# Optimization experiments

Hardware: AMD Instinct MI355X
Metric: run time of the kernel (lower is better)

## Reference

```python
import jax, jax.numpy as jnp
import numpy as np


def setup_inputs() -> dict:
    key = jax.random.key(0)
    ks = jax.random.split(key, 12)
    B, T, E, H, D, NB, BS = 64, 1, 1280, 20, 64, 7, 64
    w = lambda k: jax.random.normal(k, (E, E), jnp.float32) * 0.02
    return {
        "hidden_states": jax.random.normal(ks[0], (B, T, E), jnp.float32),
        "kcache": jax.random.normal(ks[1], (B, H, NB, BS, D), jnp.float32),
        "vcache": jax.random.normal(ks[2], (B, H, NB, BS, D), jnp.float32),
        "wq": w(ks[3]), "bq": jax.random.normal(ks[4], (E,), jnp.float32) * 0.02,
        "wk": w(ks[5]), "bk": jnp.zeros((E,), jnp.float32),
        "wv": w(ks[6]), "bv": jax.random.normal(ks[7], (E,), jnp.float32) * 0.02,
        "wo": w(ks[8]), "bo": jax.random.normal(ks[9], (E,), jnp.float32) * 0.02,
        "cache_position": jax.random.randint(ks[10], (B,), 0, 447, jnp.int32),
        "block_tables": jax.random.randint(ks[11], (B, NB), 0, NB, jnp.int32),
    }


def reference(hidden_states, kcache, vcache, wq, bq, wk, bk, wv, bv, wo, bo,
              cache_position, block_tables):
    B, T, E = hidden_states.shape          # T == 1 (decode)
    _, H, NB, BS, D = kcache.shape
    L = NB * BS                             # max logical cache length (448)
    scaling = D ** -0.5

    # projections -> (B, H, T, D)
    q = (hidden_states @ wq.T + bq).reshape(B, T, H, D).transpose(0, 2, 1, 3) * scaling
    kn = (hidden_states @ wk.T + bk).reshape(B, T, H, D).transpose(0, 2, 1, 3)
    vn = (hidden_states @ wv.T + bv).reshape(B, T, H, D).transpose(0, 2, 1, 3)

    # paged block-table gather: logical cache (B, H, L, D)
    bt = block_tables[:, None, :, None, None].astype(jnp.int32)
    kc = jnp.take_along_axis(kcache, bt, axis=2).reshape(B, H, L, D)
    vc = jnp.take_along_axis(vcache, bt, axis=2).reshape(B, H, L, D)

    # insert the new token's k/v at position cache_position[b]
    pos = jnp.arange(L, dtype=jnp.int32)
    seq = cache_position.reshape(B, 1, 1, 1)
    at_new = pos.reshape(1, 1, L, 1) == seq          # (B,1,L,1)
    k_full = jnp.where(at_new, kn, kc)               # kn (B,H,1,D) broadcasts
    v_full = jnp.where(at_new, vn, vc)

    # causal decode: attend to positions <= cache_position
    scores = jnp.einsum('bhtd,bhld->bhtl', q, k_full)
    valid = pos.reshape(1, 1, 1, L) <= cache_position.reshape(B, 1, 1, 1)
    scores = jnp.where(valid, scores, jnp.finfo(scores.dtype).min)
    probs = jax.nn.softmax(scores, axis=-1)
    out = jnp.einsum('bhtl,bhld->bhtd', probs, v_full)

    out = out.transpose(0, 2, 1, 3).reshape(B, T, E)
    return out @ wo.T + bo
```

## Files before the change

kernel.cpp:

```cpp
#include <hip/hip_runtime.h>
#include <math.h>

#define E 1280
#define NHEAD 20
#define HD 64
#define NBLK 7
#define NB 64

typedef __bf16 bf16x8 __attribute__((ext_vector_type(8)));
typedef __bf16 bf16x4 __attribute__((ext_vector_type(4)));
typedef float floatx4 __attribute__((ext_vector_type(4)));

__device__ __forceinline__ float wave_max64(float v) {
    #pragma unroll
    for (int o = 32; o > 0; o >>= 1) v = fmaxf(v, __shfl_xor(v, o, 64));
    return v;
}
__device__ __forceinline__ float wave_sum64(float v) {
    #pragma unroll
    for (int o = 32; o > 0; o >>= 1) v += __shfl_xor(v, o, 64);
    return v;
}

__device__ __forceinline__ bf16x4 cvt4(float4 v) {
    bf16x4 p;
    p[0] = (__bf16)v.x; p[1] = (__bf16)v.y; p[2] = (__bf16)v.z; p[3] = (__bf16)v.w;
    return p;
}

template<int NTOT, bool QKV>
__global__ __launch_bounds__(256) void mfma_gemm(
    const float* __restrict__ A,
    const float* __restrict__ W0, const float* __restrict__ W1,
    const float* __restrict__ W2,
    const float* __restrict__ b0, const float* __restrict__ b1,
    const float* __restrict__ b2,
    float* __restrict__ C)
{
    __shared__ __align__(16) __bf16 Asl[4][64][72];
    __shared__ __align__(16) __bf16 Wsl[4][16][72];

    const int t = threadIdx.x;
    const int lane = t & 63;
    const int wv = t >> 6;
    const int quad = lane >> 4;
    const int l16 = lane & 15;
    const int jg0 = blockIdx.x * 16;

    int j0; const float* Wp; const float* bp; float scl;
    if (QKV) {
        const int msel = jg0 / E;
        j0 = jg0 - msel * E;
        Wp = (msel == 0) ? W0 : ((msel == 1) ? W1 : W2);
        bp = (msel == 0) ? b0 : ((msel == 1) ? b1 : b2);
        scl = (msel == 0) ? 0.125f : 1.0f;
    } else { j0 = jg0; Wp = W0; bp = b0; scl = 1.0f; }

    const int sr = lane >> 2;
    const int sc = lane & 3;

    floatx4 acc[4] = {};

    const int kbeg = wv * (E / 4);
    for (int c = 0; c < 5; ++c) {
        const int k0 = kbeg + c * 64;
        #pragma unroll
        for (int rg = 0; rg < 4; ++rg) {
            #pragma unroll
            for (int cg = 0; cg < 4; ++cg) {
                float4 v = *(const float4*)&A[(size_t)(rg * 16 + sr) * E + k0 + cg * 16 + sc * 4];
                *(bf16x4*)&Asl[wv][rg * 16 + sr][cg * 16 + sc * 4] = cvt4(v);
            }
        }
        #pragma unroll
        for (int cg = 0; cg < 4; ++cg) {
            float4 v = *(const float4*)&Wp[(size_t)(j0 + sr) * E + k0 + cg * 16 + sc * 4];
            *(bf16x4*)&Wsl[wv][sr][cg * 16 + sc * 4] = cvt4(v);
        }
        bf16x8 bfr0 = *(const bf16x8*)&Wsl[wv][l16][quad * 8];
        bf16x8 bfr1 = *(const bf16x8*)&Wsl[wv][l16][32 + quad * 8];
        #pragma unroll
        for (int rg = 0; rg < 4; ++rg) {
            bf16x8 af0 = *(const bf16x8*)&Asl[wv][rg * 16 + l16][quad * 8];
            acc[rg] = __builtin_amdgcn_mfma_f32_16x16x32_bf16(af0, bfr0, acc[rg], 0, 0, 0);
            bf16x8 af1 = *(const bf16x8*)&Asl[wv][rg * 16 + l16][32 + quad * 8];
            acc[rg] = __builtin_amdgcn_mfma_f32_16x16x32_bf16(af1, bfr1, acc[rg], 0, 0, 0);
        }
    }

    __syncthreads();
    float (*Cred)[64][16] = (float (*)[64][16])&Asl[0][0][0];
    #pragma unroll
    for (int r = 0; r < 4; ++r) {
        #pragma unroll
        for (int rg = 0; rg < 4; ++rg)
            ;
        ;
    }
    #pragma unroll
    for (int rg = 0; rg < 4; ++rg) {
        #pragma unroll
        for (int r = 0; r < 4; ++r)
            Cred[wv][rg * 16 + quad * 4 + r][l16] = acc[rg][r];
    }
    __syncthreads();

    #pragma unroll
    for (int i = 0; i < 4; ++i) {
        const int e = t + i * 256;
        const int row = e >> 4, col = e & 15;
        float s = Cred[0][row][col] + Cred[1][row][col]
                + Cred[2][row][col] + Cred[3][row][col];
        C[(size_t)row * NTOT + jg0 + col] = (s + bp[j0 + col]) * scl;
    }
}

__global__ __launch_bounds__(256) void attn_kernel(
    const float* __restrict__ qkv,
    const float* __restrict__ kcache, const float* __restrict__ vcache,
    const int* __restrict__ cache_position, const int* __restrict__ block_tables,
    float* __restrict__ obuf)
{
    const int bh = blockIdx.x;
    const int b = bh / NHEAD;
    const int h = bh % NHEAD;
    const int lane = threadIdx.x & 63;
    const int wv = threadIdx.x >> 6;
    const int d4 = lane & 15;
    const int sg = lane >> 4;

    __shared__ __align__(16) float q_lds[64];
    __shared__ __align__(16) float o_lds[4][64];
    __shared__ float ml_lds[4][2];

    const int pos = cache_position[b];
    const int last = pos - 1;
    const int col = h * HD + lane;

    const float qd  = qkv[(size_t)b * (3 * E) + col];
    const float knd = qkv[(size_t)b * (3 * E) + E + col];
    const float vnd = qkv[(size_t)b * (3 * E) + 2 * E + col];
    if (wv == 0) q_lds[lane] = qd;
    __syncthreads();

    float m = -INFINITY, lsum = 0.0f;
    float4 vacc = make_float4(0.f, 0.f, 0.f, 0.f);

    for (int nb = wv; nb * 64 <= last; nb += 4) {
        const int phys = block_tables[b * NBLK + nb];
        const size_t boff = ((size_t)((b * NHEAD + h) * NBLK + phys)) << 12;
        const float* __restrict__ Kb = kcache + boff;
        const float* __restrict__ Vb = vcache + boff;

        float sc = 0.0f;
        const float4* Krow = (const float4*)(Kb + lane * HD);
        #pragma unroll
        for (int dd = 0; dd < 16; ++dd) {
            float4 k4 = Krow[dd];
            float4 q4 = ((const float4*)q_lds)[dd];
            sc = fmaf(k4.x, q4.x, sc);
            sc = fmaf(k4.y, q4.y, sc);
            sc = fmaf(k4.z, q4.z, sc);
            sc = fmaf(k4.w, q4.w, sc);
        }
        const int l = nb * 64 + lane;
        if (l > last) sc = -INFINITY;

        const float bm = wave_max64(sc);
        const float mnew = fmaxf(m, bm);
        const float alpha = __expf(m - mnew);
        const float p = __expf(sc - mnew);
        lsum = lsum * alpha + wave_sum64(p);
        vacc.x *= alpha; vacc.y *= alpha; vacc.z *= alpha; vacc.w *= alpha;

        #pragma unroll
        for (int j = 0; j < 16; ++j) {
            const int s = sg + 4 * j;
            const float ps = __shfl(p, s, 64);
            float4 v4 = *(const float4*)&Vb[s * HD + d4 * 4];
            vacc.x = fmaf(ps, v4.x, vacc.x);
            vacc.y = fmaf(ps, v4.y, vacc.y);
            vacc.z = fmaf(ps, v4.z, vacc.z);
            vacc.w = fmaf(ps, v4.w, vacc.w);
        }
        m = mnew;
    }

    #pragma unroll
    for (int o = 16; o <= 32; o <<= 1) {
        vacc.x += __shfl_xor(vacc.x, o, 64);
        vacc.y += __shfl_xor(vacc.y, o, 64);
        vacc.z += __shfl_xor(vacc.z, o, 64);
        vacc.w += __shfl_xor(vacc.w, o, 64);
    }
    if (sg == 0) *(float4*)&o_lds[wv][d4 * 4] = vacc;
    if (lane == 0) { ml_lds[wv][0] = m; ml_lds[wv][1] = lsum; }
    __syncthreads();

    if (wv == 0) {
        const float qk = wave_sum64(qd * knd);
        float Mf = qk;
        #pragma unroll
        for (int w = 0; w < 4; ++w) Mf = fmaxf(Mf, ml_lds[w][0]);
        float osum = 0.0f, Ls = 0.0f;
        #pragma unroll
        for (int w = 0; w < 4; ++w) {
            const float f = __expf(ml_lds[w][0] - Mf);
            osum = fmaf(o_lds[w][lane], f, osum);
            Ls   = fmaf(ml_lds[w][1], f, Ls);
        }
        const float pn = __expf(qk - Mf);
        osum = fmaf(pn, vnd, osum);
        Ls += pn;
        obuf[(size_t)b * E + h * HD + lane] = osum / Ls;
    }
}

extern "C" void kernel_launch(void* const* d_in, const int* in_sizes, int n_in,
                              void* d_out, int out_size, void* d_ws, size_t ws_size,
                              hipStream_t stream) {
    const float* hidden = (const float*)d_in[0];
    const float* kcache = (const float*)d_in[1];
    const float* vcache = (const float*)d_in[2];
    const float* wq = (const float*)d_in[3];
    const float* bq = (const float*)d_in[4];
    const float* wk = (const float*)d_in[5];
    const float* bk = (const float*)d_in[6];
    const float* wvp = (const float*)d_in[7];
    const float* bv = (const float*)d_in[8];
    const float* wo = (const float*)d_in[9];
    const float* bo = (const float*)d_in[10];
    const int* cpos = (const int*)d_in[11];
    const int* btab = (const int*)d_in[12];
    float* out = (float*)d_out;

    float* ws = (float*)d_ws;
    float* qkv = ws;
    float* ob  = ws + 64 * 3 * E;

    mfma_gemm<3 * E, true><<<(3 * E) / 16, 256, 0, stream>>>(
        hidden, wq, wk, wvp, bq, bk, bv, qkv);
    attn_kernel<<<NB * NHEAD, 256, 0, stream>>>(qkv, kcache, vcache, cpos, btab, ob);
    mfma_gemm<E, false><<<E / 16, 256, 0, stream>>>(
        ob, wo, wo, wo, bo, bo, bo, out);
}
```

Before: 337.5 us.

## Fuse QKV, attention and output projection into one cooperative persistent kernel

Replaces the three separate launches with a single cooperative kernel of 512 blocks. Grid-wide syncs separate the QKV GEMM, attention and O-projection phases, and the original separate kernels remain as a fallback if the cooperative launch fails. The GEMM tile loader also gains register double-buffering, prefetching the next K-chunk of A and W before the current chunk is converted and multiplied. The aim is to remove launch gaps and hide global load latency. The cost is grid-sync overhead, idle blocks in the GEMM phases, and more register pressure under launch_bounds(256,2).

```diff
diff --git a/kernel.cpp b/kernel.cpp
--- a/kernel.cpp
+++ b/kernel.cpp
@@ -1,41 +1,42 @@
 #include <hip/hip_runtime.h>
+#include <hip/hip_cooperative_groups.h>
 #include <math.h>
 
 #define E 1280
 #define NHEAD 20
 #define HD 64
 #define NBLK 7
-#define NB 64
+#define NBATCH 64
+#define GRID 512
+#define NTILE_QKV (3 * E / 16)
+#define NTILE_O   (E / 16)
+
+namespace cg = cooperative_groups;
 
 typedef __bf16 bf16x8 __attribute__((ext_vector_type(8)));
 typedef __bf16 bf16x4 __attribute__((ext_vector_type(4)));
 typedef float floatx4 __attribute__((ext_vector_type(4)));
 
 __device__ __forceinline__ float wave_max64(float v) {
-    #pragma unroll
+#pragma unroll
     for (int o = 32; o > 0; o >>= 1) v = fmaxf(v, __shfl_xor(v, o, 64));
     return v;
 }
 __device__ __forceinline__ float wave_sum64(float v) {
-    #pragma unroll
+#pragma unroll
     for (int o = 32; o > 0; o >>= 1) v += __shfl_xor(v, o, 64);
     return v;
 }
-
 __device__ __forceinline__ bf16x4 cvt4(float4 v) {
     bf16x4 p;
     p[0] = (__bf16)v.x; p[1] = (__bf16)v.y; p[2] = (__bf16)v.z; p[3] = (__bf16)v.w;
     return p;
 }
 
-template<int NTOT, bool QKV>
-__global__ __launch_bounds__(256) void mfma_gemm(
-    const float* __restrict__ A,
-    const float* __restrict__ W0, const float* __restrict__ W1,
-    const float* __restrict__ W2,
-    const float* __restrict__ b0, const float* __restrict__ b1,
-    const float* __restrict__ b2,
-    float* __restrict__ C)
+__device__ __forceinline__ void gemm_tile(
+    const float* __restrict__ A, const float* __restrict__ Wp,
+    const float* __restrict__ bp, const float scl,
+    const int j0, const int jg0, const int ldC, float* __restrict__ C)
 {
     __shared__ __align__(16) __bf16 Asl[4][64][72];
     __shared__ __align__(16) __bf16 Wsl[4][16][72];
@@ -45,93 +46,113 @@
     const int wv = t >> 6;
     const int quad = lane >> 4;
     const int l16 = lane & 15;
-    const int jg0 = blockIdx.x * 16;
-
-    int j0; const float* Wp; const float* bp; float scl;
-    if (QKV) {
-        const int msel = jg0 / E;
-        j0 = jg0 - msel * E;
-        Wp = (msel == 0) ? W0 : ((msel == 1) ? W1 : W2);
-        bp = (msel == 0) ? b0 : ((msel == 1) ? b1 : b2);
-        scl = (msel == 0) ? 0.125f : 1.0f;
-    } else { j0 = jg0; Wp = W0; bp = b0; scl = 1.0f; }
-
     const int sr = lane >> 2;
     const int sc = lane & 3;
 
     floatx4 acc[4] = {};
-
     const int kbeg = wv * (E / 4);
+
+    float4 Ab[16], Wb[4];
+#pragma unroll
+    for (int rg = 0; rg < 4; ++rg)
+#pragma unroll
+        for (int cg = 0; cg < 4; ++cg)
+            Ab[rg * 4 + cg] = *(const float4*)&A[(size_t)(rg * 16 + sr) * E + kbeg + cg * 16 + sc * 4];
+#pragma unroll
+    for (int cg = 0; cg < 4; ++cg)
+        Wb[cg] = *(const float4*)&Wp[(size_t)(j0 + sr) * E + kbeg + cg * 16 + sc * 4];
+
+#pragma unroll
     for (int c = 0; c < 5; ++c) {
-        const int k0 = kbeg + c * 64;
-        #pragma unroll
-        for (int rg = 0; rg < 4; ++rg) {
-            #pragma unroll
-            for (int cg = 0; cg < 4; ++cg) {
-                float4 v = *(const float4*)&A[(size_t)(rg * 16 + sr) * E + k0 + cg * 16 + sc * 4];
-                *(bf16x4*)&Asl[wv][rg * 16 + sr][cg * 16 + sc * 4] = cvt4(v);
-            }
-        }
-        #pragma unroll
-        for (int cg = 0; cg < 4; ++cg) {
-            float4 v = *(const float4*)&Wp[(size_t)(j0 + sr) * E + k0 + cg * 16 + sc * 4];
-            *(bf16x4*)&Wsl[wv][sr][cg * 16 + sc * 4] = cvt4(v);
-        }
+        float4 An[16], Wn[4];
+        if (c < 4) {
+            const int k1 = kbeg + (c + 1) * 64;
+#pragma unroll
+            for (int rg = 0; rg < 4; ++rg)
+#pragma unroll
+                for (int cg = 0; cg < 4; ++cg)
+                    An[rg * 4 + cg] = *(const float4*)&A[(size_t)(rg * 16 + sr) * E + k1 + cg * 16 + sc * 4];
+#pragma unroll
+            for (int cg = 0; cg < 4; ++cg)
+                Wn[cg] = *(const float4*)&Wp[(size_t)(j0 + sr) * E + k1 + cg * 16 + sc * 4];
+        }
+#pragma unroll
+        for (int rg = 0; rg < 4; ++rg)
+#pragma unroll
+            for (int cg = 0; cg < 4; ++cg)
+                *(bf16x4*)&Asl[wv][rg * 16 + sr][cg * 16 + sc * 4] = cvt4(Ab[rg * 4 + cg]);
+#pragma unroll
+        for (int cg = 0; cg < 4; ++cg)
+            *(bf16x4*)&Wsl[wv][sr][cg * 16 + sc * 4] = cvt4(Wb[cg]);
+
         bf16x8 bfr0 = *(const bf16x8*)&Wsl[wv][l16][quad * 8];
         bf16x8 bfr1 = *(const bf16x8*)&Wsl[wv][l16][32 + quad * 8];
-        #pragma unroll
+#pragma unroll
         for (int rg = 0; rg < 4; ++rg) {
             bf16x8 af0 = *(const bf16x8*)&Asl[wv][rg * 16 + l16][quad * 8];
             acc[rg] = __builtin_amdgcn_mfma_f32_16x16x32_bf16(af0, bfr0, acc[rg], 0, 0, 0);
             bf16x8 af1 = *(const bf16x8*)&Asl[wv][rg * 16 + l16][32 + quad * 8];
             acc[rg] = __builtin_amdgcn_mfma_f32_16x16x32_bf16(af1, bfr1, acc[rg], 0, 0, 0);
         }
+        if (c < 4) {
+#pragma unroll
+            for (int i = 0; i < 16; ++i) Ab[i] = An[i];
+#pragma unroll
+            for (int i = 0; i < 4; ++i) Wb[i] = Wn[i];
+        }
     }
 
     __syncthreads();
     float (*Cred)[64][16] = (float (*)[64][16])&Asl[0][0][0];
-    #pragma unroll
-    for (int r = 0; r < 4; ++r) {
-        #pragma unroll
-        for (int rg = 0; rg < 4; ++rg)
-            ;
-        ;
-    }
-    #pragma unroll
-    for (int rg = 0; rg < 4; ++rg) {
-        #pragma unroll
+#pragma unroll
+    for (int rg = 0; rg < 4; ++rg)
+#pragma unroll
         for (int r = 0; r < 4; ++r)
             Cred[wv][rg * 16 + quad * 4 + r][l16] = acc[rg][r];
-    }
-    __syncthreads();
-
-    #pragma unroll
+    __syncthreads();
+#pragma unroll
     for (int i = 0; i < 4; ++i) {
         const int e = t + i * 256;
         const int row = e >> 4, col = e & 15;
         float s = Cred[0][row][col] + Cred[1][row][col]
                 + Cred[2][row][col] + Cred[3][row][col];
-        C[(size_t)row * NTOT + jg0 + col] = (s + bp[j0 + col]) * scl;
-    }
-}
-
-__global__ __launch_bounds__(256) void attn_kernel(
-    const float* __restrict__ qkv,
+        C[(size_t)row * ldC + jg0 + col] = (s + bp[j0 + col]) * scl;
+    }
+    __syncthreads();
+}
+
+__device__ __forceinline__ void qkv_tile(
+    const int tile, const float* __restrict__ hidden,
+    const float* __restrict__ wq, const float* __restrict__ bq,
+    const float* __restrict__ wk, const float* __restrict__ bk,
+    const float* __restrict__ wv_, const float* __restrict__ bv,
+    float* __restrict__ qkv)
+{
+    const int jg0 = tile * 16;
+    const int msel = jg0 / E;
+    const int j0 = jg0 - msel * E;
+    const float* Wp = (msel == 0) ? wq : ((msel == 1) ? wk : wv_);
+    const float* bp = (msel == 0) ? bq : ((msel == 1) ? bk : bv);
+    const float scl = (msel == 0) ? 0.125f : 1.0f;
+    gemm_tile(hidden, Wp, bp, scl, j0, jg0, 3 * E, qkv);
+}
+
+__device__ __forceinline__ void attn_unit(
+    const int bh, const float* __restrict__ qkv,
     const float* __restrict__ kcache, const float* __restrict__ vcache,
     const int* __restrict__ cache_position, const int* __restrict__ block_tables,
     float* __restrict__ obuf)
 {
-    const int bh = blockIdx.x;
+    __shared__ __align__(16) float q_lds[64];
+    __shared__ __align__(16) float o_lds[4][64];
+    __shared__ float ml_lds[4][2];
+
     const int b = bh / NHEAD;
-    const int h = bh % NHEAD;
+    const int h = bh - b * NHEAD;
     const int lane = threadIdx.x & 63;
     const int wv = threadIdx.x >> 6;
     const int d4 = lane & 15;
     const int sg = lane >> 4;
-
-    __shared__ __align__(16) float q_lds[64];
-    __shared__ __align__(16) float o_lds[4][64];
-    __shared__ float ml_lds[4][2];
 
     const int pos = cache_position[b];
     const int last = pos - 1;
@@ -154,7 +175,7 @@
 
         float sc = 0.0f;
         const float4* Krow = (const float4*)(Kb + lane * HD);
-        #pragma unroll
+#pragma unroll
         for (int dd = 0; dd < 16; ++dd) {
             float4 k4 = Krow[dd];
             float4 q4 = ((const float4*)q_lds)[dd];
@@ -173,7 +194,7 @@
         lsum = lsum * alpha + wave_sum64(p);
         vacc.x *= alpha; vacc.y *= alpha; vacc.z *= alpha; vacc.w *= alpha;
 
-        #pragma unroll
+#pragma unroll
         for (int j = 0; j < 16; ++j) {
             const int s = sg + 4 * j;
             const float ps = __shfl(p, s, 64);
@@ -186,7 +207,7 @@
         m = mnew;
     }
 
-    #pragma unroll
+#pragma unroll
     for (int o = 16; o <= 32; o <<= 1) {
         vacc.x += __shfl_xor(vacc.x, o, 64);
         vacc.y += __shfl_xor(vacc.y, o, 64);
@@ -200,10 +221,10 @@
     if (wv == 0) {
         const float qk = wave_sum64(qd * knd);
         float Mf = qk;
-        #pragma unroll
+#pragma unroll
         for (int w = 0; w < 4; ++w) Mf = fmaxf(Mf, ml_lds[w][0]);
         float osum = 0.0f, Ls = 0.0f;
-        #pragma unroll
+#pragma unroll
         for (int w = 0; w < 4; ++w) {
             const float f = __expf(ml_lds[w][0] - Mf);
             osum = fmaf(o_lds[w][lane], f, osum);
@@ -214,6 +235,61 @@
         Ls += pn;
         obuf[(size_t)b * E + h * HD + lane] = osum / Ls;
     }
+    __syncthreads();
+}
+
+__global__ __launch_bounds__(256, 2) void fused_kernel(
+    const float* __restrict__ hidden,
+    const float* __restrict__ kcache, const float* __restrict__ vcache,
+    const float* __restrict__ wq, const float* __restrict__ bq,
+    const float* __restrict__ wk, const float* __restrict__ bk,
+    const float* __restrict__ wv_, const float* __restrict__ bv,
+    const float* __restrict__ wo, const float* __restrict__ bo,
+    const int* __restrict__ cpos, const int* __restrict__ btab,
+    float* __restrict__ out, float* __restrict__ qkv, float* __restrict__ ob)
+{
+    const int bb = blockIdx.x;
+    cg::grid_group grid = cg::this_grid();
+
+    if (bb < NTILE_QKV)
+        qkv_tile(bb, hidden, wq, bq, wk, bk, wv_, bv, qkv);
+
+    __threadfence();
+    grid.sync();
+
+    for (int u = bb; u < NBATCH * NHEAD; u += GRID)
+        attn_unit(u, qkv, kcache, vcache, cpos, btab, ob);
+
+    __threadfence();
+    grid.sync();
+
+    if (bb < NTILE_O)
+        gemm_tile(ob, wo, bo, 1.0f, bb * 16, bb * 16, E, out);
+}
+
+__global__ __launch_bounds__(256) void qkv_kernel_sep(
+    const float* __restrict__ hidden,
+    const float* __restrict__ wq, const float* __restrict__ bq,
+    const float* __restrict__ wk, const float* __restrict__ bk,
+    const float* __restrict__ wv_, const float* __restrict__ bv,
+    float* __restrict__ qkv)
+{
+    qkv_tile(blockIdx.x, hidden, wq, bq, wk, bk, wv_, bv, qkv);
+}
+__global__ __launch_bounds__(256) void attn_kernel_sep(
+    const float* __restrict__ qkv,
+    const float* __restrict__ kcache, const float* __restrict__ vcache,
+    const int* __restrict__ cpos, const int* __restrict__ btab,
+    float* __restrict__ ob)
+{
+    attn_unit(blockIdx.x, qkv, kcache, vcache, cpos, btab, ob);
+}
+__global__ __launch_bounds__(256) void oproj_kernel_sep(
+    const float* __restrict__ ob,
+    const float* __restrict__ wo, const float* __restrict__ bo,
+    float* __restrict__ out)
+{
+    gemm_tile(ob, wo, bo, 1.0f, blockIdx.x * 16, blockIdx.x * 16, E, out);
 }
 
 extern "C" void kernel_launch(void* const* d_in, const int* in_sizes, int n_in,
@@ -238,9 +314,18 @@
     float* qkv = ws;
     float* ob  = ws + 64 * 3 * E;
 
-    mfma_gemm<3 * E, true><<<(3 * E) / 16, 256, 0, stream>>>(
-        hidden, wq, wk, wvp, bq, bk, bv, qkv);
-    attn_kernel<<<NB * NHEAD, 256, 0, stream>>>(qkv, kcache, vcache, cpos, btab, ob);
-    mfma_gemm<E, false><<<E / 16, 256, 0, stream>>>(
-        ob, wo, wo, wo, bo, bo, bo, out);
-}
+    void* args[16] = {
+        (void*)&hidden, (void*)&kcache, (void*)&vcache,
+        (void*)&wq, (void*)&bq, (void*)&wk, (void*)&bk,
+        (void*)&wvp, (void*)&bv, (void*)&wo, (void*)&bo,
+        (void*)&cpos, (void*)&btab, (void*)&out, (void*)&qkv, (void*)&ob
+    };
+    hipError_t err = hipLaunchCooperativeKernel(
+        (const void*)fused_kernel, dim3(GRID), dim3(256), args, 0, stream);
+    if (err != hipSuccess) {
+        (void)hipGetLastError();
+        qkv_kernel_sep<<<NTILE_QKV, 256, 0, stream>>>(hidden, wq, bq, wk, bk, wvp, bv, qkv);
+        attn_kernel_sep<<<NBATCH * NHEAD, 256, 0, stream>>>(qkv, kcache, vcache, cpos, btab, ob);
+        oproj_kernel_sep<<<NTILE_O, 256, 0, stream>>>(ob, wo, bo, out);
+    }
+}
```

Result: slower. 585.0 us (+73.3%).

## Load GEMM operands directly into registers with prefetch; unroll attention block loop

Applied to the files above, without the earlier changes.

The GEMM no longer stages A and W tiles through shared memory. Each lane loads its MFMA fragments straight from global memory into registers, converts them to bf16 there, and prefetches the next k-chunk while the current one is computed. The attention kernel replaces its online-softmax loop with a fixed two-block-per-wave path. It issues both K dot products and the first V block loads up front, then uses a single max and sum reduction. This cuts LDS traffic and serialized loop dependencies, at the cost of much higher register pressure.

```diff
diff --git a/kernel.cpp b/kernel.cpp
--- a/kernel.cpp
+++ b/kernel.cpp
@@ -5,27 +5,26 @@
 #define NHEAD 20
 #define HD 64
 #define NBLK 7
-#define NB 64
+#define NBATCH 64
 
 typedef __bf16 bf16x8 __attribute__((ext_vector_type(8)));
-typedef __bf16 bf16x4 __attribute__((ext_vector_type(4)));
 typedef float floatx4 __attribute__((ext_vector_type(4)));
 
 __device__ __forceinline__ float wave_max64(float v) {
-    #pragma unroll
+#pragma unroll
     for (int o = 32; o > 0; o >>= 1) v = fmaxf(v, __shfl_xor(v, o, 64));
     return v;
 }
 __device__ __forceinline__ float wave_sum64(float v) {
-    #pragma unroll
+#pragma unroll
     for (int o = 32; o > 0; o >>= 1) v += __shfl_xor(v, o, 64);
     return v;
 }
-
-__device__ __forceinline__ bf16x4 cvt4(float4 v) {
-    bf16x4 p;
-    p[0] = (__bf16)v.x; p[1] = (__bf16)v.y; p[2] = (__bf16)v.z; p[3] = (__bf16)v.w;
-    return p;
+__device__ __forceinline__ bf16x8 cvt8(float4 lo, float4 hi) {
+    bf16x8 r;
+    r[0] = (__bf16)lo.x; r[1] = (__bf16)lo.y; r[2] = (__bf16)lo.z; r[3] = (__bf16)lo.w;
+    r[4] = (__bf16)hi.x; r[5] = (__bf16)hi.y; r[6] = (__bf16)hi.z; r[7] = (__bf16)hi.w;
+    return r;
 }
 
 template<int NTOT, bool QKV>
@@ -37,8 +36,7 @@
     const float* __restrict__ b2,
     float* __restrict__ C)
 {
-    __shared__ __align__(16) __bf16 Asl[4][64][72];
-    __shared__ __align__(16) __bf16 Wsl[4][16][72];
+    __shared__ __align__(16) float Cred[4][64][16];
 
     const int t = threadIdx.x;
     const int lane = t & 63;
@@ -56,56 +54,75 @@
         scl = (msel == 0) ? 0.125f : 1.0f;
     } else { j0 = jg0; Wp = W0; bp = b0; scl = 1.0f; }
 
-    const int sr = lane >> 2;
-    const int sc = lane & 3;
+    const int kbeg = wv * (E / 4);
+    const int ko = quad * 8;
+
+    const float* __restrict__ wrow = Wp + (size_t)(j0 + l16) * E;
+    const float* __restrict__ arow = A + (size_t)l16 * E;
 
     floatx4 acc[4] = {};
-
-    const int kbeg = wv * (E / 4);
+    float4 Ac[16], Wc[4];
+
+    {
+        const int k0 = kbeg;
+#pragma unroll
+        for (int rg = 0; rg < 4; ++rg) {
+            const float* ar = arow + (size_t)rg * 16 * E + k0 + ko;
+            Ac[rg * 4 + 0] = *(const float4*)(ar);
+            Ac[rg * 4 + 1] = *(const float4*)(ar + 4);
+            Ac[rg * 4 + 2] = *(const float4*)(ar + 32);
+            Ac[rg * 4 + 3] = *(const float4*)(ar + 36);
+        }
+        const float* wr = wrow + k0 + ko;
+        Wc[0] = *(const float4*)(wr);
+        Wc[1] = *(const float4*)(wr + 4);
+        Wc[2] = *(const float4*)(wr + 32);
+        Wc[3] = *(const float4*)(wr + 36);
+    }
+
+#pragma unroll
     for (int c = 0; c < 5; ++c) {
-        const int k0 = kbeg + c * 64;
-        #pragma unroll
+        float4 An[16], Wn[4];
+        if (c < 4) {
+            const int k1 = kbeg + (c + 1) * 64;
+#pragma unroll
+            for (int rg = 0; rg < 4; ++rg) {
+                const float* ar = arow + (size_t)rg * 16 * E + k1 + ko;
+                An[rg * 4 + 0] = *(const float4*)(ar);
+                An[rg * 4 + 1] = *(const float4*)(ar + 4);
+                An[rg * 4 + 2] = *(const float4*)(ar + 32);
+                An[rg * 4 + 3] = *(const float4*)(ar + 36);
+            }
+            const float* wr = wrow + k1 + ko;
+            Wn[0] = *(const float4*)(wr);
+            Wn[1] = *(const float4*)(wr + 4);
+            Wn[2] = *(const float4*)(wr + 32);
+            Wn[3] = *(const float4*)(wr + 36);
+        }
+        const bf16x8 bf0 = cvt8(Wc[0], Wc[1]);
+        const bf16x8 bf1 = cvt8(Wc[2], Wc[3]);
+#pragma unroll
         for (int rg = 0; rg < 4; ++rg) {
-            #pragma unroll
-            for (int cg = 0; cg < 4; ++cg) {
-                float4 v = *(const float4*)&A[(size_t)(rg * 16 + sr) * E + k0 + cg * 16 + sc * 4];
-                *(bf16x4*)&Asl[wv][rg * 16 + sr][cg * 16 + sc * 4] = cvt4(v);
-            }
-        }
-        #pragma unroll
-        for (int cg = 0; cg < 4; ++cg) {
-            float4 v = *(const float4*)&Wp[(size_t)(j0 + sr) * E + k0 + cg * 16 + sc * 4];
-            *(bf16x4*)&Wsl[wv][sr][cg * 16 + sc * 4] = cvt4(v);
-        }
-        bf16x8 bfr0 = *(const bf16x8*)&Wsl[wv][l16][quad * 8];
-        bf16x8 bfr1 = *(const bf16x8*)&Wsl[wv][l16][32 + quad * 8];
-        #pragma unroll
-        for (int rg = 0; rg < 4; ++rg) {
-            bf16x8 af0 = *(const bf16x8*)&Asl[wv][rg * 16 + l16][quad * 8];
-            acc[rg] = __builtin_amdgcn_mfma_f32_16x16x32_bf16(af0, bfr0, acc[rg], 0, 0, 0);
-            bf16x8 af1 = *(const bf16x8*)&Asl[wv][rg * 16 + l16][32 + quad * 8];
-            acc[rg] = __builtin_amdgcn_mfma_f32_16x16x32_bf16(af1, bfr1, acc[rg], 0, 0, 0);
-        }
-    }
-
-    __syncthreads();
-    float (*Cred)[64][16] = (float (*)[64][16])&Asl[0][0][0];
-    #pragma unroll
-    for (int r = 0; r < 4; ++r) {
-        #pragma unroll
-        for (int rg = 0; rg < 4; ++rg)
-            ;
-        ;
-    }
-    #pragma unroll
-    for (int rg = 0; rg < 4; ++rg) {
-        #pragma unroll
+            acc[rg] = __builtin_amdgcn_mfma_f32_16x16x32_bf16(
+                cvt8(Ac[rg * 4 + 0], Ac[rg * 4 + 1]), bf0, acc[rg], 0, 0, 0);
+            acc[rg] = __builtin_amdgcn_mfma_f32_16x16x32_bf16(
+                cvt8(Ac[rg * 4 + 2], Ac[rg * 4 + 3]), bf1, acc[rg], 0, 0, 0);
+        }
+        if (c < 4) {
+#pragma unroll
+            for (int i = 0; i < 16; ++i) Ac[i] = An[i];
+#pragma unroll
+            for (int i = 0; i < 4; ++i) Wc[i] = Wn[i];
+        }
+    }
+
+#pragma unroll
+    for (int rg = 0; rg < 4; ++rg)
+#pragma unroll
         for (int r = 0; r < 4; ++r)
             Cred[wv][rg * 16 + quad * 4 + r][l16] = acc[rg][r];
-    }
     __syncthreads();
-
-    #pragma unroll
+#pragma unroll
     for (int i = 0; i < 4; ++i) {
         const int e = t + i * 256;
         const int row = e >> 4, col = e & 15;
@@ -123,7 +140,7 @@
 {
     const int bh = blockIdx.x;
     const int b = bh / NHEAD;
-    const int h = bh % NHEAD;
+    const int h = bh - b * NHEAD;
     const int lane = threadIdx.x & 63;
     const int wv = threadIdx.x >> 6;
     const int d4 = lane & 15;
@@ -146,47 +163,87 @@
     float m = -INFINITY, lsum = 0.0f;
     float4 vacc = make_float4(0.f, 0.f, 0.f, 0.f);
 
-    for (int nb = wv; nb * 64 <= last; nb += 4) {
-        const int phys = block_tables[b * NBLK + nb];
-        const size_t boff = ((size_t)((b * NHEAD + h) * NBLK + phys)) << 12;
-        const float* __restrict__ Kb = kcache + boff;
-        const float* __restrict__ Vb = vcache + boff;
-
-        float sc = 0.0f;
-        const float4* Krow = (const float4*)(Kb + lane * HD);
-        #pragma unroll
-        for (int dd = 0; dd < 16; ++dd) {
-            float4 k4 = Krow[dd];
-            float4 q4 = ((const float4*)q_lds)[dd];
-            sc = fmaf(k4.x, q4.x, sc);
-            sc = fmaf(k4.y, q4.y, sc);
-            sc = fmaf(k4.z, q4.z, sc);
-            sc = fmaf(k4.w, q4.w, sc);
-        }
-        const int l = nb * 64 + lane;
-        if (l > last) sc = -INFINITY;
-
-        const float bm = wave_max64(sc);
-        const float mnew = fmaxf(m, bm);
-        const float alpha = __expf(m - mnew);
-        const float p = __expf(sc - mnew);
-        lsum = lsum * alpha + wave_sum64(p);
-        vacc.x *= alpha; vacc.y *= alpha; vacc.z *= alpha; vacc.w *= alpha;
-
-        #pragma unroll
+    const int nb0 = wv;
+    const int nb1 = wv + 4;
+    const bool hasb0 = (nb0 * 64 <= last);
+    const bool hasb1 = (nb1 * 64 <= last);
+
+    if (hasb0) {
+        const size_t bhoff = (size_t)(b * NHEAD + h) * NBLK;
+        const int phys0 = block_tables[b * NBLK + nb0];
+        const float* __restrict__ Kb0 = kcache + ((bhoff + phys0) << 12);
+        const float* __restrict__ Vb0 = vcache + ((bhoff + phys0) << 12);
+        const float* __restrict__ Kb1 = Kb0;
+        const float* __restrict__ Vb1 = Vb0;
+        if (hasb1) {
+            const int phys1 = block_tables[b * NBLK + nb1];
+            Kb1 = kcache + ((bhoff + phys1) << 12);
+            Vb1 = vcache + ((bhoff + phys1) << 12);
+        }
+
+        float sc0 = 0.0f, sc1 = -INFINITY;
+        {
+            const float4* Krow = (const float4*)(Kb0 + lane * HD);
+#pragma unroll
+            for (int dd = 0; dd < 16; ++dd) {
+                float4 k4 = Krow[dd];
+                float4 q4 = ((const float4*)q_lds)[dd];
+                sc0 = fmaf(k4.x, q4.x, sc0);
+                sc0 = fmaf(k4.y, q4.y, sc0);
+                sc0 = fmaf(k4.z, q4.z, sc0);
+                sc0 = fmaf(k4.w, q4.w, sc0);
+            }
+            if (nb0 * 64 + lane > last) sc0 = -INFINITY;
+        }
+        if (hasb1) {
+            float s1 = 0.0f;
+            const float4* Krow = (const float4*)(Kb1 + lane * HD);
+#pragma unroll
+            for (int dd = 0; dd < 16; ++dd) {
+                float4 k4 = Krow[dd];
+                float4 q4 = ((const float4*)q_lds)[dd];
+                s1 = fmaf(k4.x, q4.x, s1);
+                s1 = fmaf(k4.y, q4.y, s1);
+                s1 = fmaf(k4.z, q4.z, s1);
+                s1 = fmaf(k4.w, q4.w, s1);
+            }
+            sc1 = (nb1 * 64 + lane > last) ? -INFINITY : s1;
+        }
+
+        float4 v0r[16];
+#pragma unroll
+        for (int j = 0; j < 16; ++j)
+            v0r[j] = *(const float4*)&Vb0[(sg + 4 * j) * HD + d4 * 4];
+
+        const float m_ = wave_max64(fmaxf(sc0, sc1));
+        const float p0 = __expf(sc0 - m_);
+        const float p1 = __expf(sc1 - m_);
+        lsum = wave_sum64(p0 + p1);
+        m = m_;
+
+#pragma unroll
         for (int j = 0; j < 16; ++j) {
-            const int s = sg + 4 * j;
-            const float ps = __shfl(p, s, 64);
-            float4 v4 = *(const float4*)&Vb[s * HD + d4 * 4];
-            vacc.x = fmaf(ps, v4.x, vacc.x);
-            vacc.y = fmaf(ps, v4.y, vacc.y);
-            vacc.z = fmaf(ps, v4.z, vacc.z);
-            vacc.w = fmaf(ps, v4.w, vacc.w);
-        }
-        m = mnew;
-    }
-
-    #pragma unroll
+            const float ps = __shfl(p0, sg + 4 * j, 64);
+            vacc.x = fmaf(ps, v0r[j].x, vacc.x);
+            vacc.y = fmaf(ps, v0r[j].y, vacc.y);
+            vacc.z = fmaf(ps, v0r[j].z, vacc.z);
+            vacc.w = fmaf(ps, v0r[j].w, vacc.w);
+        }
+        if (hasb1) {
+#pragma unroll
+            for (int j = 0; j < 16; ++j) {
+                const int s = sg + 4 * j;
+                const float ps = __shfl(p1, s, 64);
+                float4 v4 = *(const float4*)&Vb1[s * HD + d4 * 4];
+                vacc.x = fmaf(ps, v4.x, vacc.x);
+                vacc.y = fmaf(ps, v4.y, vacc.y);
+                vacc.z = fmaf(ps, v4.z, vacc.z);
+                vacc.w = fmaf(ps, v4.w, vacc.w);
+            }
+        }
+    }
+
+#pragma unroll
     for (int o = 16; o <= 32; o <<= 1) {
         vacc.x += __shfl_xor(vacc.x, o, 64);
         vacc.y += __shfl_xor(vacc.y, o, 64);
@@ -200,10 +257,10 @@
     if (wv == 0) {
         const float qk = wave_sum64(qd * knd);
         float Mf = qk;
-        #pragma unroll
+#pragma unroll
         for (int w = 0; w < 4; ++w) Mf = fmaxf(Mf, ml_lds[w][0]);
         float osum = 0.0f, Ls = 0.0f;
-        #pragma unroll
+#pragma unroll
         for (int w = 0; w < 4; ++w) {
             const float f = __expf(ml_lds[w][0] - Mf);
             osum = fmaf(o_lds[w][lane], f, osum);
@@ -240,7 +297,7 @@
 
     mfma_gemm<3 * E, true><<<(3 * E) / 16, 256, 0, stream>>>(
         hidden, wq, wk, wvp, bq, bk, bv, qkv);
-    attn_kernel<<<NB * NHEAD, 256, 0, stream>>>(qkv, kcache, vcache, cpos, btab, ob);
+    attn_kernel<<<NBATCH * NHEAD, 256, 0, stream>>>(qkv, kcache, vcache, cpos, btab, ob);
     mfma_gemm<E, false><<<E / 16, 256, 0, stream>>>(
         ob, wo, wo, wo, bo, bo, bo, out);
 }
```

Result: faster. 326.3 us (-3.3%).
